# Optimization experiments

Hardware: AMD Instinct MI355X
Metric: run time of the kernel (lower is better)

## Reference

```python
import jax, jax.numpy as jnp
import numpy as np
from jax import lax

CHUNK = 256  # query chunk size (manual tiling block)

def setup_inputs() -> dict:
    key = jax.random.key(0)
    kq, kk, kv = jax.random.split(key, 3)
    shape = (2, 16, 2048, 128)  # [B, H, S, D]
    q = jax.random.normal(kq, shape, dtype=jnp.float32)
    k = jax.random.normal(kk, shape, dtype=jnp.float32)
    v = jax.random.normal(kv, shape, dtype=jnp.float32)
    return {"q": q, "k": k, "v": v}

def reference(q, k, v):
    # Chunked (memory-efficient) exact attention: softmax(QK^T/sqrt(D)) V,
    # computed one query block at a time so the full [S,S] score matrix
    # is never materialized.
    B, H, S, D = q.shape
    scale = jnp.asarray(1.0 / np.sqrt(D), dtype=q.dtype)
    n_chunks = S // CHUNK
    # [n_chunks, B, H, CHUNK, D]
    q_blocks = q.reshape(B, H, n_chunks, CHUNK, D).transpose(2, 0, 1, 3, 4)

    def step(carry, q_blk):
        # scores for this query block vs all keys: [B, H, CHUNK, S]
        s = jnp.einsum('bhqd,bhkd->bhqk', q_blk, k) * scale
        p = jax.nn.softmax(s, axis=-1)
        o = jnp.einsum('bhqk,bhkd->bhqd', p, v)
        return carry, o

    _, out_blocks = lax.scan(step, None, q_blocks)
    # [n_chunks, B, H, CHUNK, D] -> [B, H, S, D]
    out = out_blocks.transpose(1, 2, 0, 3, 4).reshape(B, H, S, D)
    return out
```

## Files before the change

### kernel.cpp

```cpp
#include <hip/hip_runtime.h>
#include <hip/hip_bf16.h>


typedef short short8 __attribute__((ext_vector_type(8)));
typedef float f32x16 __attribute__((ext_vector_type(16)));

#define MFMA32(a, b, c) __builtin_amdgcn_mfma_f32_32x32x16_bf16((a), (b), (c), 0, 0, 0)

#if __has_builtin(__builtin_amdgcn_exp2f)
#define EXP2(x) __builtin_amdgcn_exp2f(x)
#else
#define EXP2(x) exp2f(x)
#endif

constexpr int Dh  = 128;
constexpr int S_  = 2048;
constexpr int KVB = 64;
constexpr int NT  = S_ / KVB;
constexpr int WAVES = 4;
constexpr int QBLK  = 128;

__device__ __forceinline__ short f2bf(float f) {
    union { float f; unsigned u; } x; x.f = f;
    unsigned r = x.u + 0x7fffu + ((x.u >> 16) & 1u);
    return (short)(r >> 16);
}

__device__ __forceinline__ unsigned pkbf(float lo, float hi) {
    unsigned r;
    asm("v_cvt_pk_bf16_f32 %0, %1, %2" : "=v"(r) : "v"(lo), "v"(hi));
    return r;
}

__device__ __forceinline__ void pswap(unsigned &a, unsigned &b) {
    asm("v_permlane32_swap_b32 %0, %1" : "+v"(a), "+v"(b));
}

__device__ __forceinline__ void gload16(const void* g, void* l) {
    __builtin_amdgcn_global_load_lds(
        (const __attribute__((address_space(1))) unsigned int*)g,
        (__attribute__((address_space(3))) unsigned int*)l, 16, 0, 0);
}

__global__ __launch_bounds__(256) void prep_kv(const float* __restrict__ K,
                                               const float* __restrict__ V,
                                               short* __restrict__ Kz,
                                               short* __restrict__ Vt) {
    __shared__ short tr[64][132];
    if (blockIdx.x < 4096) {
        int idx = blockIdx.x * 256 + threadIdx.x;
        int b   = idx & 15;
        int s   = (idx >> 4) & (S_ - 1);
        int sb  = b ^ (s & 15);
        const float* src = K + (size_t)(idx >> 4) * Dh + sb * 8;
        float4 f0 = ((const float4*)src)[0];
        float4 f1 = ((const float4*)src)[1];
        short8 o;
        o[0] = f2bf(f0.x); o[1] = f2bf(f0.y); o[2] = f2bf(f0.z); o[3] = f2bf(f0.w);
        o[4] = f2bf(f1.x); o[5] = f2bf(f1.y); o[6] = f2bf(f1.z); o[7] = f2bf(f1.w);
        *(short8*)(Kz + (size_t)idx * 8) = o;
    } else {
        int bid = blockIdx.x - 4096;
        int seg = bid & 31, bh = bid >> 5;
        int t = threadIdx.x;
        {
            const int s = t >> 2, d0 = (t & 3) * 32;
            const float* src = V + ((size_t)(bh * S_ + seg * 64 + s)) * Dh + d0;
            #pragma unroll
            for (int i = 0; i < 4; ++i) {
                float4 f0 = ((const float4*)src)[2 * i];
                float4 f1 = ((const float4*)src)[2 * i + 1];
                short8 o;
                o[0] = f2bf(f0.x); o[1] = f2bf(f0.y); o[2] = f2bf(f0.z); o[3] = f2bf(f0.w);
                o[4] = f2bf(f1.x); o[5] = f2bf(f1.y); o[6] = f2bf(f1.z); o[7] = f2bf(f1.w);
                *(short8*)&tr[s][d0 + i * 8] = o;
            }
        }
        __syncthreads();
        short* outb = Vt + ((size_t)(bh * 32 + seg)) * 8192;
        #pragma unroll
        for (int jj = 0; jj < 4; ++jj) {
            const int j   = (t << 2) | jj;
            const int dt  = j >> 8;
            const int ks  = (j >> 6) & 3;
            const int ln  = j & 63;
            const int hi2 = ln >> 5, l31 = ln & 31;
            short8 o;
            #pragma unroll
            for (int e = 0; e < 8; ++e)
                o[e] = tr[ks * 16 + hi2 * 8 + e][dt * 32 + l31];
            *(short8*)(outb + (size_t)j * 8) = o;
        }
    }
}

__global__ __launch_bounds__(256, 2)
void mea_fwd11(const float* __restrict__ Qg, const short* __restrict__ Kz,
               const short* __restrict__ Vt, float* __restrict__ Og, int nqt) {
    __shared__ __align__(16) short k0[KVB * Dh], k1[KVB * Dh];
    __shared__ float bc_lds[WAVES][32];

    const int bid = blockIdx.x;
    const int cpx = (int)gridDim.x >> 3;
    const int swz = (bid & 7) * cpx + (bid >> 3);
    const int qt  = swz % nqt;
    const int bh  = swz / nqt;

    const int tid  = threadIdx.x;
    const int w    = tid >> 6;
    const int lane = tid & 63;
    const int l31  = lane & 31;
    const int hi   = lane >> 5;

    const size_t base = (size_t)bh * S_ * Dh;
    const int    qrow = qt * QBLK + w * 32 + l31;
    const float  QSC  = 0.08838834764831845f * 1.4426950408889634f;

    short8 qf[8];
    {
        const float* qp = Qg + base + (size_t)qrow * Dh;
        #pragma unroll
        for (int kc = 0; kc < 8; ++kc) {
            const float4 f0 = *(const float4*)(qp + kc * 16 + hi * 8);
            const float4 f1 = *(const float4*)(qp + kc * 16 + hi * 8 + 4);
            short8 a;
            a[0] = f2bf(f0.x * QSC); a[1] = f2bf(f0.y * QSC);
            a[2] = f2bf(f0.z * QSC); a[3] = f2bf(f0.w * QSC);
            a[4] = f2bf(f1.x * QSC); a[5] = f2bf(f1.y * QSC);
            a[6] = f2bf(f1.z * QSC); a[7] = f2bf(f1.w * QSC);
            qf[kc] = a;
        }
    }

    f32x16 oacc[4];
    #pragma unroll
    for (int dt = 0; dt < 4; ++dt)
        #pragma unroll
        for (int r = 0; r < 16; ++r) oacc[dt][r] = 0.f;
    float mrun = -1e30f, lpart = 0.f;

    const short* kt0 = Kz + base;
    const short* vt0 = Vt + base;

    auto STAGE = [&](short* kl, int t) {
        const short* ks = kt0 + (size_t)t * (KVB * Dh);
        #pragma unroll
        for (int i = 0; i < 4; ++i) {
            const int ou = (i * 4 + w) * 512;
            gload16(ks + ou + lane * 8, kl + ou);
        }
    };

#define VLD(vg, dt, ks) (*(const short8*)((vg) + (((dt) * 4 + (ks)) * 64 + lane) * 8))

    auto COMPUTE = [&](const short* kl, int t) {
        const short* vg = vt0 + (size_t)t * 8192;

        f32x16 SA, SB;
        #pragma unroll
        for (int r = 0; r < 16; ++r) { SA[r] = 0.f; SB[r] = 0.f; }
        __builtin_amdgcn_s_setprio(1);
        #pragma unroll
        for (int kc = 0; kc < 8; ++kc) {
            const int go = (((kc * 2 + hi) ^ (l31 & 15)) * 8);
            const short8 a0 = *(const short8*)&kl[l31 * Dh + go];
            const short8 a1 = *(const short8*)&kl[(32 + l31) * Dh + go];
            SA = MFMA32(a0, qf[kc], SA);
            SB = MFMA32(a1, qf[kc], SB);
        }
        __builtin_amdgcn_s_setprio(0);

        short8 x0 = VLD(vg, 0, 0), x1 = VLD(vg, 0, 1);
        short8 x2 = VLD(vg, 0, 2), x3 = VLD(vg, 0, 3);

        float mxl = SA[0];
        #pragma unroll
        for (int r = 1; r < 16; ++r) mxl = fmaxf(mxl, SA[r]);
        #pragma unroll
        for (int r = 0; r < 16; ++r) mxl = fmaxf(mxl, SB[r]);
        if (__any(mxl > mrun + 8.0f)) {
            float mo   = fmaxf(mxl, __shfl_xor(mxl, 32));
            float mnew = fmaxf(mrun, mo);
            float rc   = EXP2(mrun - mnew);
            mrun = mnew;
            lpart *= rc;
            if (!hi) bc_lds[w][l31] = rc;
            #pragma unroll
            for (int m = 0; m < 4; ++m) {
                const float4 rcv = *(const float4*)&bc_lds[w][m * 8 + 4 * hi];
                #pragma unroll
                for (int t2 = 0; t2 < 4; ++t2) {
                    const float f = (&rcv.x)[t2];
                    #pragma unroll
                    for (int dt = 0; dt < 4; ++dt) oacc[dt][m * 4 + t2] *= f;
                }
            }
        }

        float sum = 0.f;
        #pragma unroll
        for (int r = 0; r < 16; ++r) { SA[r] = EXP2(SA[r] - mrun); sum += SA[r]; }
        #pragma unroll
        for (int r = 0; r < 16; ++r) { SB[r] = EXP2(SB[r] - mrun); sum += SB[r]; }
        lpart += sum;

        short8 pf[4];
        #pragma unroll
        for (int kk = 0; kk < 2; ++kk) {
            unsigned a0 = pkbf(SA[kk * 8 + 0], SA[kk * 8 + 1]);
            unsigned a1 = pkbf(SA[kk * 8 + 2], SA[kk * 8 + 3]);
            unsigned b0 = pkbf(SA[kk * 8 + 4], SA[kk * 8 + 5]);
            unsigned b1 = pkbf(SA[kk * 8 + 6], SA[kk * 8 + 7]);
            pswap(a0, b0); pswap(a1, b1);
            unsigned wd[4] = {a0, a1, b0, b1};
            pf[kk] = *(const short8*)wd;
        }
        #pragma unroll
        for (int kk = 0; kk < 2; ++kk) {
            unsigned a0 = pkbf(SB[kk * 8 + 0], SB[kk * 8 + 1]);
            unsigned a1 = pkbf(SB[kk * 8 + 2], SB[kk * 8 + 3]);
            unsigned b0 = pkbf(SB[kk * 8 + 4], SB[kk * 8 + 5]);
            unsigned b1 = pkbf(SB[kk * 8 + 6], SB[kk * 8 + 7]);
            pswap(a0, b0); pswap(a1, b1);
            unsigned wd[4] = {a0, a1, b0, b1};
            pf[2 + kk] = *(const short8*)wd;
        }

        short8 w0 = VLD(vg, 1, 0), w1 = VLD(vg, 1, 1);
        short8 w2 = VLD(vg, 1, 2), w3 = VLD(vg, 1, 3);
        __builtin_amdgcn_s_setprio(1);
        oacc[0] = MFMA32(pf[0], x0, oacc[0]); oacc[0] = MFMA32(pf[1], x1, oacc[0]);
        oacc[0] = MFMA32(pf[2], x2, oacc[0]); oacc[0] = MFMA32(pf[3], x3, oacc[0]);
        __builtin_amdgcn_s_setprio(0);
        x0 = VLD(vg, 2, 0); x1 = VLD(vg, 2, 1);
        x2 = VLD(vg, 2, 2); x3 = VLD(vg, 2, 3);
        __builtin_amdgcn_s_setprio(1);
        oacc[1] = MFMA32(pf[0], w0, oacc[1]); oacc[1] = MFMA32(pf[1], w1, oacc[1]);
        oacc[1] = MFMA32(pf[2], w2, oacc[1]); oacc[1] = MFMA32(pf[3], w3, oacc[1]);
        __builtin_amdgcn_s_setprio(0);
        w0 = VLD(vg, 3, 0); w1 = VLD(vg, 3, 1);
        w2 = VLD(vg, 3, 2); w3 = VLD(vg, 3, 3);
        __builtin_amdgcn_s_setprio(1);
        oacc[2] = MFMA32(pf[0], x0, oacc[2]); oacc[2] = MFMA32(pf[1], x1, oacc[2]);
        oacc[2] = MFMA32(pf[2], x2, oacc[2]); oacc[2] = MFMA32(pf[3], x3, oacc[2]);
        oacc[3] = MFMA32(pf[0], w0, oacc[3]); oacc[3] = MFMA32(pf[1], w1, oacc[3]);
        oacc[3] = MFMA32(pf[2], w2, oacc[3]); oacc[3] = MFMA32(pf[3], w3, oacc[3]);
        __builtin_amdgcn_s_setprio(0);
    };

    STAGE(k0, 0);
    __syncthreads();
    #pragma unroll 1
    for (int t = 0; t < NT; t += 2) {
        STAGE(k1, t + 1);
        COMPUTE(k0, t);
        __syncthreads();
        if (t + 2 < NT) STAGE(k0, t + 2);
        COMPUTE(k1, t + 1);
        __syncthreads();
    }

    {
        const float tot = lpart + __shfl_xor(lpart, 32);
        if (!hi) bc_lds[w][l31] = 1.0f / tot;
    }
    float* op = Og + base;
    #pragma unroll
    for (int m = 0; m < 4; ++m) {
        const float4 li = *(const float4*)&bc_lds[w][m * 8 + 4 * hi];
        #pragma unroll
        for (int t2 = 0; t2 < 4; ++t2) {
            const int row  = m * 8 + 4 * hi + t2;
            const float lf = (&li.x)[t2];
            #pragma unroll
            for (int dt = 0; dt < 4; ++dt)
                op[(size_t)(qt * QBLK + w * 32 + row) * Dh + dt * 32 + l31]
                    = oacc[dt][m * 4 + t2] * lf;
        }
    }
#undef VLD
}

typedef float f32x4 __attribute__((ext_vector_type(4)));
#define MFMA16(a, b, c) __builtin_amdgcn_mfma_f32_16x16x32_bf16((a), (b), (c), 0, 0, 0)
constexpr int FKVB = 32;
constexpr int FKP  = 136;
constexpr int FVP  = 40;
constexpr int FPP  = 40;

__global__ __launch_bounds__(256, 2)
void mea_fwd_fb(const float* __restrict__ Qg, const float* __restrict__ Kg,
                const float* __restrict__ Vg, float* __restrict__ Og,
                int S, int nqt) {
    __shared__ __align__(16) short k_lds[FKVB][FKP];
    __shared__ __align__(16) short vT_lds[Dh][FVP];
    __shared__ __align__(16) short p_lds[4][16][FPP];

    const int qt = blockIdx.x % nqt;
    const int bh = blockIdx.x / nqt;
    const int tid = threadIdx.x;
    const int w = tid >> 6, lane = tid & 63;
    const int lr = lane & 15, lg = lane >> 4;
    const size_t base = (size_t)bh * S * Dh;
    const int qrow0 = qt * 64 + w * 16;
    const float scale = 0.08838834764831845f;

    short8 qf[4];
    {
        const float* qp = Qg + base + (size_t)(qrow0 + lr) * Dh;
        #pragma unroll
        for (int kc = 0; kc < 4; ++kc) {
            const float4 f0 = *(const float4*)(qp + kc * 32 + lg * 8);
            const float4 f1 = *(const float4*)(qp + kc * 32 + lg * 8 + 4);
            short8 a;
            a[0] = f2bf(f0.x); a[1] = f2bf(f0.y); a[2] = f2bf(f0.z); a[3] = f2bf(f0.w);
            a[4] = f2bf(f1.x); a[5] = f2bf(f1.y); a[6] = f2bf(f1.z); a[7] = f2bf(f1.w);
            qf[kc] = a;
        }
    }
    f32x4 oacc[8];
    #pragma unroll
    for (int dt = 0; dt < 8; ++dt) oacc[dt] = (f32x4){0.f, 0.f, 0.f, 0.f};
    float mrun[4] = {-1e30f, -1e30f, -1e30f, -1e30f};
    float lrun[4] = {0.f, 0.f, 0.f, 0.f};
    const int sr = tid >> 3, sc = (tid & 7) * 16;

    for (int kv0 = 0; kv0 < S; kv0 += FKVB) {
        {
            const float* kp = Kg + base + (size_t)(kv0 + sr) * Dh + sc;
            const float* vp = Vg + base + (size_t)(kv0 + sr) * Dh + sc;
            short8 pk0, pk1;
            float4 f0 = ((const float4*)kp)[0], f1 = ((const float4*)kp)[1];
            float4 f2 = ((const float4*)kp)[2], f3 = ((const float4*)kp)[3];
            pk0[0] = f2bf(f0.x); pk0[1] = f2bf(f0.y); pk0[2] = f2bf(f0.z); pk0[3] = f2bf(f0.w);
            pk0[4] = f2bf(f1.x); pk0[5] = f2bf(f1.y); pk0[6] = f2bf(f1.z); pk0[7] = f2bf(f1.w);
            pk1[0] = f2bf(f2.x); pk1[1] = f2bf(f2.y); pk1[2] = f2bf(f2.z); pk1[3] = f2bf(f2.w);
            pk1[4] = f2bf(f3.x); pk1[5] = f2bf(f3.y); pk1[6] = f2bf(f3.z); pk1[7] = f2bf(f3.w);
            *(short8*)&k_lds[sr][sc] = pk0;
            *(short8*)&k_lds[sr][sc + 8] = pk1;
            #pragma unroll
            for (int i = 0; i < 4; ++i) {
                float4 f = ((const float4*)vp)[i];
                vT_lds[sc + 4 * i + 0][sr] = f2bf(f.x);
                vT_lds[sc + 4 * i + 1][sr] = f2bf(f.y);
                vT_lds[sc + 4 * i + 2][sr] = f2bf(f.z);
                vT_lds[sc + 4 * i + 3][sr] = f2bf(f.w);
            }
        }
        __syncthreads();
        f32x4 s0 = (f32x4){0.f,0.f,0.f,0.f}, s1 = (f32x4){0.f,0.f,0.f,0.f};
        #pragma unroll
        for (int kc = 0; kc < 4; ++kc) {
            short8 b0 = *(const short8*)&k_lds[lr][kc * 32 + lg * 8];
            short8 b1 = *(const short8*)&k_lds[16 + lr][kc * 32 + lg * 8];
            s0 = MFMA16(qf[kc], b0, s0);
            s1 = MFMA16(qf[kc], b1, s1);
        }
        float resc[4];
        #pragma unroll
        for (int r = 0; r < 4; ++r) {
            float mxv = fmaxf(s0[r], s1[r]);
            #pragma unroll
            for (int m = 1; m < 16; m <<= 1) mxv = fmaxf(mxv, __shfl_xor(mxv, m));
            float mnew = fmaxf(mrun[r], mxv * scale);
            float rc = __expf(mrun[r] - mnew);
            mrun[r] = mnew;
            float p0 = __expf(s0[r] * scale - mnew);
            float p1 = __expf(s1[r] * scale - mnew);
            float rs = p0 + p1;
            #pragma unroll
            for (int m = 1; m < 16; m <<= 1) rs += __shfl_xor(rs, m);
            lrun[r] = lrun[r] * rc + rs;
            resc[r] = rc;
            p_lds[w][lg * 4 + r][lr] = f2bf(p0);
            p_lds[w][lg * 4 + r][16 + lr] = f2bf(p1);
        }
        #pragma unroll
        for (int dt = 0; dt < 8; ++dt) {
            f32x4 o = oacc[dt];
            o[0] *= resc[0]; o[1] *= resc[1]; o[2] *= resc[2]; o[3] *= resc[3];
            oacc[dt] = o;
        }
        short8 ap = *(const short8*)&p_lds[w][lr][lg * 8];
        #pragma unroll
        for (int dt = 0; dt < 8; ++dt) {
            short8 bv = *(const short8*)&vT_lds[dt * 16 + lr][lg * 8];
            oacc[dt] = MFMA16(ap, bv, oacc[dt]);
        }
        __syncthreads();
    }
    float inv[4];
    #pragma unroll
    for (int r = 0; r < 4; ++r) inv[r] = 1.0f / lrun[r];
    float* op = Og + base;
    #pragma unroll
    for (int dt = 0; dt < 8; ++dt)
        #pragma unroll
        for (int r = 0; r < 4; ++r)
            op[(size_t)(qrow0 + lg * 4 + r) * Dh + dt * 16 + lr] = oacc[dt][r] * inv[r];
}

extern "C" void kernel_launch(void* const* d_in, const int* in_sizes, int n_in,
                              void* d_out, int out_size, void* d_ws, size_t ws_size,
                              hipStream_t stream) {
    const float* q = (const float*)d_in[0];
    const float* k = (const float*)d_in[1];
    const float* v = (const float*)d_in[2];
    float* o = (float*)d_out;

    const int BH  = in_sizes[0] / (S_ * Dh);
    const int nqt = S_ / QBLK;

    const size_t kz_bytes = (size_t)BH * S_ * Dh * sizeof(short);
    const size_t need = 2 * kz_bytes;

    if (ws_size >= need) {
        short* Kz = (short*)d_ws;
        short* Vt = (short*)((char*)d_ws + kz_bytes);
        hipLaunchKernelGGL(prep_kv, dim3(4096 + BH * 32), dim3(256),
                           0, stream, k, v, Kz, Vt);
        hipLaunchKernelGGL(mea_fwd11, dim3(BH * nqt), dim3(256), 0, stream,
                           q, Kz, Vt, o, nqt);
    } else {
        hipLaunchKernelGGL(mea_fwd_fb, dim3(BH * (S_ / 64)), dim3(256), 0, stream,
                           q, k, v, o, S_, S_ / 64);
    }
}
```

Measured before the change: 102.8 us.

## Split KV sequence in two per query tile and merge partials in combine kernel

Adds a split-K (flash-decoding style) path: each query tile is processed by two blocks, each covering half of the key/value sequence, which write unnormalized partial outputs plus row max and sum to workspace. A new combine kernel rescales and merges the two partials into the final output. This doubles the grid (512 → 1024 blocks) to improve CU occupancy and tail balance on the 256-CU device, at the cost of extra fp32 partial-output traffic, a third launch, and duplicated Q loading.

```diff
diff --git a/kernel.cpp b/kernel.cpp
--- a/kernel.cpp
+++ b/kernel.cpp
@@ -17,6 +17,7 @@
 constexpr int S_  = 2048;
 constexpr int KVB = 64;
 constexpr int NT  = S_ / KVB;
+constexpr int NT2 = NT / 2;
 constexpr int WAVES = 4;
 constexpr int QBLK  = 128;
 
@@ -95,16 +96,19 @@
 }
 
 __global__ __launch_bounds__(256, 2)
-void mea_fwd11(const float* __restrict__ Qg, const short* __restrict__ Kz,
-               const short* __restrict__ Vt, float* __restrict__ Og, int nqt) {
+void mea_fwd12(const float* __restrict__ Qg, const short* __restrict__ Kz,
+               const short* __restrict__ Vt, float* __restrict__ Opart,
+               float* __restrict__ Mlp, int nqt) {
     __shared__ __align__(16) short k0[KVB * Dh], k1[KVB * Dh];
     __shared__ float bc_lds[WAVES][32];
 
     const int bid = blockIdx.x;
     const int cpx = (int)gridDim.x >> 3;
     const int swz = (bid & 7) * cpx + (bid >> 3);
-    const int qt  = swz % nqt;
-    const int bh  = swz / nqt;
+    const int qth = swz % (nqt * 2);
+    const int bh  = swz / (nqt * 2);
+    const int qt  = qth >> 1;
+    const int h   = qth & 1;
 
     const int tid  = threadIdx.x;
     const int w    = tid >> 6;
@@ -139,8 +143,9 @@
         for (int r = 0; r < 16; ++r) oacc[dt][r] = 0.f;
     float mrun = -1e30f, lpart = 0.f;
 
-    const short* kt0 = Kz + base;
-    const short* vt0 = Vt + base;
+    const size_t hoff = (size_t)h * NT2 * (KVB * Dh);
+    const short* kt0 = Kz + base + hoff;
+    const short* vt0 = Vt + base + hoff;
 
     auto STAGE = [&](short* kl, int t) {
         const short* ks = kt0 + (size_t)t * (KVB * Dh);
@@ -156,6 +161,228 @@
     auto COMPUTE = [&](const short* kl, int t) {
         const short* vg = vt0 + (size_t)t * 8192;
 
+        f32x16 SA, SB;
+        #pragma unroll
+        for (int r = 0; r < 16; ++r) { SA[r] = 0.f; SB[r] = 0.f; }
+        __builtin_amdgcn_s_setprio(1);
+        #pragma unroll
+        for (int kc = 0; kc < 8; ++kc) {
+            const int go = (((kc * 2 + hi) ^ (l31 & 15)) * 8);
+            const short8 a0 = *(const short8*)&kl[l31 * Dh + go];
+            const short8 a1 = *(const short8*)&kl[(32 + l31) * Dh + go];
+            SA = MFMA32(a0, qf[kc], SA);
+            SB = MFMA32(a1, qf[kc], SB);
+        }
+        __builtin_amdgcn_s_setprio(0);
+
+        short8 x0 = VLD(vg, 0, 0), x1 = VLD(vg, 0, 1);
+        short8 x2 = VLD(vg, 0, 2), x3 = VLD(vg, 0, 3);
+
+        float mxl = SA[0];
+        #pragma unroll
+        for (int r = 1; r < 16; ++r) mxl = fmaxf(mxl, SA[r]);
+        #pragma unroll
+        for (int r = 0; r < 16; ++r) mxl = fmaxf(mxl, SB[r]);
+        if (__any(mxl > mrun + 8.0f)) {
+            float mo   = fmaxf(mxl, __shfl_xor(mxl, 32));
+            float mnew = fmaxf(mrun, mo);
+            float rc   = EXP2(mrun - mnew);
+            mrun = mnew;
+            lpart *= rc;
+            if (!hi) bc_lds[w][l31] = rc;
+            #pragma unroll
+            for (int m = 0; m < 4; ++m) {
+                const float4 rcv = *(const float4*)&bc_lds[w][m * 8 + 4 * hi];
+                #pragma unroll
+                for (int t2 = 0; t2 < 4; ++t2) {
+                    const float f = (&rcv.x)[t2];
+                    #pragma unroll
+                    for (int dt = 0; dt < 4; ++dt) oacc[dt][m * 4 + t2] *= f;
+                }
+            }
+        }
+
+        float sum = 0.f;
+        #pragma unroll
+        for (int r = 0; r < 16; ++r) { SA[r] = EXP2(SA[r] - mrun); sum += SA[r]; }
+        #pragma unroll
+        for (int r = 0; r < 16; ++r) { SB[r] = EXP2(SB[r] - mrun); sum += SB[r]; }
+        lpart += sum;
+
+        short8 pf[4];
+        #pragma unroll
+        for (int kk = 0; kk < 2; ++kk) {
+            unsigned a0 = pkbf(SA[kk * 8 + 0], SA[kk * 8 + 1]);
+            unsigned a1 = pkbf(SA[kk * 8 + 2], SA[kk * 8 + 3]);
+            unsigned b0 = pkbf(SA[kk * 8 + 4], SA[kk * 8 + 5]);
+            unsigned b1 = pkbf(SA[kk * 8 + 6], SA[kk * 8 + 7]);
+            pswap(a0, b0); pswap(a1, b1);
+            unsigned wd[4] = {a0, a1, b0, b1};
+            pf[kk] = *(const short8*)wd;
+        }
+        #pragma unroll
+        for (int kk = 0; kk < 2; ++kk) {
+            unsigned a0 = pkbf(SB[kk * 8 + 0], SB[kk * 8 + 1]);
+            unsigned a1 = pkbf(SB[kk * 8 + 2], SB[kk * 8 + 3]);
+            unsigned b0 = pkbf(SB[kk * 8 + 4], SB[kk * 8 + 5]);
+            unsigned b1 = pkbf(SB[kk * 8 + 6], SB[kk * 8 + 7]);
+            pswap(a0, b0); pswap(a1, b1);
+            unsigned wd[4] = {a0, a1, b0, b1};
+            pf[2 + kk] = *(const short8*)wd;
+        }
+
+        short8 w0 = VLD(vg, 1, 0), w1 = VLD(vg, 1, 1);
+        short8 w2 = VLD(vg, 1, 2), w3 = VLD(vg, 1, 3);
+        __builtin_amdgcn_s_setprio(1);
+        oacc[0] = MFMA32(pf[0], x0, oacc[0]); oacc[0] = MFMA32(pf[1], x1, oacc[0]);
+        oacc[0] = MFMA32(pf[2], x2, oacc[0]); oacc[0] = MFMA32(pf[3], x3, oacc[0]);
+        __builtin_amdgcn_s_setprio(0);
+        x0 = VLD(vg, 2, 0); x1 = VLD(vg, 2, 1);
+        x2 = VLD(vg, 2, 2); x3 = VLD(vg, 2, 3);
+        __builtin_amdgcn_s_setprio(1);
+        oacc[1] = MFMA32(pf[0], w0, oacc[1]); oacc[1] = MFMA32(pf[1], w1, oacc[1]);
+        oacc[1] = MFMA32(pf[2], w2, oacc[1]); oacc[1] = MFMA32(pf[3], w3, oacc[1]);
+        __builtin_amdgcn_s_setprio(0);
+        w0 = VLD(vg, 3, 0); w1 = VLD(vg, 3, 1);
+        w2 = VLD(vg, 3, 2); w3 = VLD(vg, 3, 3);
+        __builtin_amdgcn_s_setprio(1);
+        oacc[2] = MFMA32(pf[0], x0, oacc[2]); oacc[2] = MFMA32(pf[1], x1, oacc[2]);
+        oacc[2] = MFMA32(pf[2], x2, oacc[2]); oacc[2] = MFMA32(pf[3], x3, oacc[2]);
+        oacc[3] = MFMA32(pf[0], w0, oacc[3]); oacc[3] = MFMA32(pf[1], w1, oacc[3]);
+        oacc[3] = MFMA32(pf[2], w2, oacc[3]); oacc[3] = MFMA32(pf[3], w3, oacc[3]);
+        __builtin_amdgcn_s_setprio(0);
+    };
+
+    STAGE(k0, 0);
+    __syncthreads();
+    #pragma unroll 1
+    for (int t = 0; t < NT2; t += 2) {
+        STAGE(k1, t + 1);
+        COMPUTE(k0, t);
+        __syncthreads();
+        if (t + 2 < NT2) STAGE(k0, t + 2);
+        COMPUTE(k1, t + 1);
+        __syncthreads();
+    }
+
+    const int pidx = (bh * nqt + qt) * 2 + h;
+    {
+        const float tot = lpart + __shfl_xor(lpart, 32);
+        if (!hi) {
+            Mlp[(size_t)pidx * 256 + (w * 32 + l31) * 2 + 0] = mrun;
+            Mlp[(size_t)pidx * 256 + (w * 32 + l31) * 2 + 1] = tot;
+        }
+    }
+    float* op = Opart + (size_t)pidx * (QBLK * Dh);
+    #pragma unroll
+    for (int m = 0; m < 4; ++m) {
+        #pragma unroll
+        for (int t2 = 0; t2 < 4; ++t2) {
+            const int row = m * 8 + 4 * hi + t2;
+            #pragma unroll
+            for (int dt = 0; dt < 4; ++dt)
+                op[(size_t)(w * 32 + row) * Dh + dt * 32 + l31]
+                    = oacc[dt][m * 4 + t2];
+        }
+    }
+#undef VLD
+}
+
+__global__ __launch_bounds__(256) void combine2(const float* __restrict__ Opart,
+                                                const float* __restrict__ Mlp,
+                                                float* __restrict__ Og, int nqt) {
+    const int blk = blockIdx.x;
+    const int qt = blk % nqt, bh = blk / nqt;
+    const int t = threadIdx.x;
+    const int row = t >> 1;
+    const int d0  = (t & 1) * 64;
+
+    const size_t p0 = ((size_t)blk * 2 + 0);
+    const size_t p1 = ((size_t)blk * 2 + 1);
+    const float m0 = Mlp[p0 * 256 + row * 2], l0 = Mlp[p0 * 256 + row * 2 + 1];
+    const float m1 = Mlp[p1 * 256 + row * 2], l1 = Mlp[p1 * 256 + row * 2 + 1];
+    const float M  = fmaxf(m0, m1);
+    float w0 = exp2f(m0 - M), w1 = exp2f(m1 - M);
+    const float inv = 1.0f / (l0 * w0 + l1 * w1);
+    w0 *= inv; w1 *= inv;
+
+    const float* a = Opart + p0 * (QBLK * Dh) + (size_t)row * Dh + d0;
+    const float* b = Opart + p1 * (QBLK * Dh) + (size_t)row * Dh + d0;
+    float* o = Og + ((size_t)bh * S_ + (size_t)qt * QBLK + row) * Dh + d0;
+    #pragma unroll
+    for (int i = 0; i < 16; ++i) {
+        const float4 x = ((const float4*)a)[i];
+        const float4 y = ((const float4*)b)[i];
+        float4 r;
+        r.x = x.x * w0 + y.x * w1;
+        r.y = x.y * w0 + y.y * w1;
+        r.z = x.z * w0 + y.z * w1;
+        r.w = x.w * w0 + y.w * w1;
+        ((float4*)o)[i] = r;
+    }
+}
+
+__global__ __launch_bounds__(256, 2)
+void mea_fwd11(const float* __restrict__ Qg, const short* __restrict__ Kz,
+               const short* __restrict__ Vt, float* __restrict__ Og, int nqt) {
+    __shared__ __align__(16) short k0[KVB * Dh], k1[KVB * Dh];
+    __shared__ float bc_lds[WAVES][32];
+
+    const int bid = blockIdx.x;
+    const int cpx = (int)gridDim.x >> 3;
+    const int swz = (bid & 7) * cpx + (bid >> 3);
+    const int qt  = swz % nqt;
+    const int bh  = swz / nqt;
+
+    const int tid  = threadIdx.x;
+    const int w    = tid >> 6;
+    const int lane = tid & 63;
+    const int l31  = lane & 31;
+    const int hi   = lane >> 5;
+
+    const size_t base = (size_t)bh * S_ * Dh;
+    const int    qrow = qt * QBLK + w * 32 + l31;
+    const float  QSC  = 0.08838834764831845f * 1.4426950408889634f;
+
+    short8 qf[8];
+    {
+        const float* qp = Qg + base + (size_t)qrow * Dh;
+        #pragma unroll
+        for (int kc = 0; kc < 8; ++kc) {
+            const float4 f0 = *(const float4*)(qp + kc * 16 + hi * 8);
+            const float4 f1 = *(const float4*)(qp + kc * 16 + hi * 8 + 4);
+            short8 a;
+            a[0] = f2bf(f0.x * QSC); a[1] = f2bf(f0.y * QSC);
+            a[2] = f2bf(f0.z * QSC); a[3] = f2bf(f0.w * QSC);
+            a[4] = f2bf(f1.x * QSC); a[5] = f2bf(f1.y * QSC);
+            a[6] = f2bf(f1.z * QSC); a[7] = f2bf(f1.w * QSC);
+            qf[kc] = a;
+        }
+    }
+
+    f32x16 oacc[4];
+    #pragma unroll
+    for (int dt = 0; dt < 4; ++dt)
+        #pragma unroll
+        for (int r = 0; r < 16; ++r) oacc[dt][r] = 0.f;
+    float mrun = -1e30f, lpart = 0.f;
+
+    const short* kt0 = Kz + base;
+    const short* vt0 = Vt + base;
+
+    auto STAGE = [&](short* kl, int t) {
+        const short* ks = kt0 + (size_t)t * (KVB * Dh);
+        #pragma unroll
+        for (int i = 0; i < 4; ++i) {
+            const int ou = (i * 4 + w) * 512;
+            gload16(ks + ou + lane * 8, kl + ou);
+        }
+    };
+
+#define VLD(vg, dt, ks) (*(const short8*)((vg) + (((dt) * 4 + (ks)) * 64 + lane) * 8))
+
+    auto COMPUTE = [&](const short* kl, int t) {
+        const short* vg = vt0 + (size_t)t * 8192;
         f32x16 SA, SB;
         #pragma unroll
         for (int r = 0; r < 16; ++r) { SA[r] = 0.f; SB[r] = 0.f; }
@@ -412,13 +639,27 @@
     const int nqt = S_ / QBLK;
 
     const size_t kz_bytes = (size_t)BH * S_ * Dh * sizeof(short);
-    const size_t need = 2 * kz_bytes;
-
-    if (ws_size >= need) {
+    const size_t op_bytes = (size_t)BH * nqt * 2 * QBLK * Dh * 4;
+    const size_t ml_bytes = (size_t)BH * nqt * 2 * 256 * 4;
+    const size_t need_base  = 2 * kz_bytes;
+    const size_t need_split = need_base + op_bytes + ml_bytes;
+
+    if (ws_size >= need_split) {
         short* Kz = (short*)d_ws;
         short* Vt = (short*)((char*)d_ws + kz_bytes);
-        hipLaunchKernelGGL(prep_kv, dim3(4096 + BH * 32), dim3(256),
-                           0, stream, k, v, Kz, Vt);
+        float* Op = (float*)((char*)d_ws + need_base);
+        float* Ml = (float*)((char*)d_ws + need_base + op_bytes);
+        hipLaunchKernelGGL(prep_kv, dim3(4096 + BH * 32), dim3(256), 0, stream,
+                           k, v, Kz, Vt);
+        hipLaunchKernelGGL(mea_fwd12, dim3(BH * nqt * 2), dim3(256), 0, stream,
+                           q, Kz, Vt, Op, Ml, nqt);
+        hipLaunchKernelGGL(combine2, dim3(BH * nqt), dim3(256), 0, stream,
+                           Op, Ml, o, nqt);
+    } else if (ws_size >= need_base) {
+        short* Kz = (short*)d_ws;
+        short* Vt = (short*)((char*)d_ws + kz_bytes);
+        hipLaunchKernelGGL(prep_kv, dim3(4096 + BH * 32), dim3(256), 0, stream,
+                           k, v, Kz, Vt);
         hipLaunchKernelGGL(mea_fwd11, dim3(BH * nqt), dim3(256), 0, stream,
                            q, Kz, Vt, o, nqt);
     } else {
```

Result: slower. 144.0 us (+40.2%).
